# Performance work log

Measured on AMD Instinct MI355X. Metric: run time of the kernel, lower is better.

Reference implementation:

```python
import jax, jax.numpy as jnp
import numpy as np

N_NODES = 50000
N_EDGES = 600000
D_IN = 128
D_HID = 128
N_IDX = 4096


def gcn_conv(x, W, b, edge_index, num_nodes):
    """PyG GCNConv: add self loops, symmetric deg normalization, scatter-add, bias."""
    h = x @ W  # [N, D_out]
    loop = jnp.arange(num_nodes, dtype=edge_index.dtype)
    src = jnp.concatenate([edge_index[0], loop])
    dst = jnp.concatenate([edge_index[1], loop])
    deg = jax.ops.segment_sum(jnp.ones_like(dst, dtype=h.dtype), dst, num_segments=num_nodes)
    dinv = jnp.where(deg > 0, jax.lax.rsqrt(jnp.maximum(deg, 1.0)), 0.0)
    norm = dinv[src] * dinv[dst]  # [E+N]
    msgs = h[src] * norm[:, None]
    out = jax.ops.segment_sum(msgs, dst, num_segments=num_nodes)
    return out + b


def setup_inputs() -> dict:
    key = jax.random.key(0)
    ks = jax.random.split(key, 18)
    d = {
        "x": jax.random.normal(ks[0], (N_NODES, D_IN), dtype=jnp.float32),
        "syntactic_edge_index": jax.random.randint(ks[1], (2, N_EDGES), 0, N_NODES, dtype=jnp.int32),
        "sequential_edge_index": jax.random.randint(ks[2], (2, N_EDGES), 0, N_NODES, dtype=jnp.int32),
        "semantic_edge_index": jax.random.randint(ks[3], (2, N_EDGES), 0, N_NODES, dtype=jnp.int32),
        "index": jax.random.randint(ks[4], (N_IDX,), 0, N_NODES, dtype=jnp.int32),
    }
    s = 1.0 / np.sqrt(D_IN)
    names = ["syn", "seq", "sem"]
    for i, n in enumerate(names):
        d[f"w1_{n}"] = jax.random.uniform(ks[5 + i], (D_IN, D_HID), jnp.float32, -s, s)
        d[f"b1_{n}"] = jnp.zeros((D_HID,), jnp.float32)
        d[f"w2_{n}"] = jax.random.uniform(ks[8 + i], (D_HID, D_HID), jnp.float32, -s, s)
        d[f"b2_{n}"] = jnp.zeros((D_HID,), jnp.float32)
    return d


def reference(x, syntactic_edge_index, sequential_edge_index, semantic_edge_index, index,
              w1_syn, b1_syn, w1_seq, b1_seq, w1_sem, b1_sem,
              w2_syn, b2_syn, w2_seq, b2_seq, w2_sem, b2_sem):
    n = x.shape[0]
    # layer 1: three parallel GCN branches + ReLU (dropout is identity in eval mode)
    a = jax.nn.relu(gcn_conv(x, w1_syn, b1_syn, syntactic_edge_index, n))
    b = jax.nn.relu(gcn_conv(x, w1_seq, b1_seq, sequential_edge_index, n))
    c = jax.nn.relu(gcn_conv(x, w1_sem, b1_sem, semantic_edge_index, n))
    h = jnp.maximum(jnp.maximum(a, b), c)
    # layer 2
    a2 = jax.nn.relu(gcn_conv(h, w2_syn, b2_syn, syntactic_edge_index, n))
    b2 = jax.nn.relu(gcn_conv(h, w2_seq, b2_seq, sequential_edge_index, n))
    c2 = jax.nn.relu(gcn_conv(h, w2_sem, b2_sem, semantic_edge_index, n))
    out = jnp.maximum(jnp.maximum(a2, b2), c2)
    return out[index]
```

## Files before the change

kernel.cpp:

```cpp
#include <hip/hip_runtime.h>
#include <hip/hip_fp16.h>

#define NN 50000
#define NE 600000
#define NG 3
#define D  128
#define NI 4096
#define BW 1024
#define NBUCK 49
#define EPT_BIN 16
#define EPB_BIN (256 * EPT_BIN)
#define NBLK_BIN ((NE + EPB_BIN - 1) / EPB_BIN)
#define XCVT_BLKS 3125
#define WCVT_BLKS 48
#define CNT_BLKS (NBLK_BIN * NG)

typedef _Float16 half8 __attribute__((ext_vector_type(8)));
typedef _Float16 half4v __attribute__((ext_vector_type(4)));
typedef float floatx4 __attribute__((ext_vector_type(4)));

static __device__ __forceinline__ float wextract(unsigned int v) {
  unsigned short u = (unsigned short)(v >> 16);
  _Float16 h;
  __builtin_memcpy(&h, &u, 2);
  return (float)h;
}

static __device__ __forceinline__ unsigned int packsw(int s, float w) {
  _Float16 h = (_Float16)w;
  unsigned short u;
  __builtin_memcpy(&u, &h, 2);
  return (unsigned int)s | ((unsigned int)u << 16);
}


__global__ __launch_bounds__(256) void prep_kernel(
    const float* __restrict__ x, __half* __restrict__ xh,
    const float* __restrict__ W0, const float* __restrict__ W1, const float* __restrict__ W2,
    const float* __restrict__ W3, const float* __restrict__ W4, const float* __restrict__ W5,
    __half* __restrict__ Wf,
    const int* __restrict__ e0, const int* __restrict__ e1, const int* __restrict__ e2,
    int* __restrict__ bucketCnt) {
  __shared__ int cnt[NBUCK];
  int blk = blockIdx.x;
  int tid = threadIdx.x;
  if (blk < XCVT_BLKS) {
    int i = blk * 256 + tid;
    size_t base = (size_t)i * 8;
    float4 v0 = *(const float4*)&x[base];
    float4 v1 = *(const float4*)&x[base + 4];
    half8 h;
    h[0] = (_Float16)v0.x; h[1] = (_Float16)v0.y; h[2] = (_Float16)v0.z; h[3] = (_Float16)v0.w;
    h[4] = (_Float16)v1.x; h[5] = (_Float16)v1.y; h[6] = (_Float16)v1.z; h[7] = (_Float16)v1.w;
    *(half8*)&xh[base] = h;
  } else if (blk < XCVT_BLKS + WCVT_BLKS) {
    const float* Wm[6] = {W0, W1, W2, W3, W4, W5};
    int t = (blk - XCVT_BLKS) * 256 + tid;
    int mat = t >> 11;
    int fr = (t >> 6) & 31;
    int lane = t & 63;
    int tt = fr >> 2, ks = fr & 3;
    int n = tt * 16 + (lane & 15);
    int kb = ks * 32 + (lane >> 4) * 8;
    const float* W = Wm[mat];
#pragma unroll
    for (int j = 0; j < 8; j++)
      Wf[(size_t)t * 8 + j] = __float2half(W[(kb + j) * 128 + n]);
  } else {
    int cb = blk - XCVT_BLKS - WCVT_BLKS;
    int g = cb / NBLK_BIN, eb = cb % NBLK_BIN;
    const int* ei = (g == 0) ? e0 : ((g == 1) ? e1 : e2);
    if (tid < NBUCK) cnt[tid] = 0;
    __syncthreads();
    int base = eb * EPB_BIN;
#pragma unroll
    for (int i = 0; i < EPT_BIN; i++) {
      int e = base + tid + i * 256;
      if (e < NE) atomicAdd(&cnt[ei[NE + e] >> 10], 1);
    }
    __syncthreads();
    if (tid < NBUCK) atomicAdd(&bucketCnt[g * NBUCK + tid], cnt[tid]);
  }
}

__global__ void bscan_kernel(const int* __restrict__ bucketCnt, int* __restrict__ bucketBase,
                             int* __restrict__ cursor, int* __restrict__ rp) {
  int g = threadIdx.x >> 6;
  int lane = threadIdx.x & 63;
  if (g >= NG) return;
  int v = (lane < NBUCK) ? bucketCnt[g * NBUCK + lane] : 0;
  int incl = v;
#pragma unroll
  for (int off = 1; off < 64; off <<= 1) {
    int t = __shfl_up(incl, off, 64);
    if (lane >= off) incl += t;
  }
  int ex = incl - v;
  if (lane < NBUCK) {
    bucketBase[g * NBUCK + lane] = ex;
    cursor[g * NBUCK + lane] = ex;
  }
  if (lane == 0) rp[g * (NN + 1) + NN] = NE;
}

__global__ __launch_bounds__(256) void bin_kernel(const int* __restrict__ e0,
    const int* __restrict__ e1, const int* __restrict__ e2,
    int* __restrict__ cursor, unsigned int* __restrict__ binned) {
  __shared__ int cnt[4][NBUCK];
  __shared__ int base[NBUCK];
  __shared__ int woff[4][NBUCK];
  int g = blockIdx.y;
  const int* ei = (g == 0) ? e0 : ((g == 1) ? e1 : e2);
  int tid = threadIdx.x;
  int wave = tid >> 6;
  if (tid < NBUCK) { cnt[0][tid] = 0; cnt[1][tid] = 0; cnt[2][tid] = 0; cnt[3][tid] = 0; }
  __syncthreads();
  int estart = blockIdx.x * EPB_BIN;
  int src[EPT_BIN], dst[EPT_BIN], rk[EPT_BIN];
#pragma unroll
  for (int i = 0; i < EPT_BIN; i++) {
    int e = estart + tid + i * 256;
    if (e < NE) {
      src[i] = ei[e];
      dst[i] = ei[NE + e];
      rk[i] = atomicAdd(&cnt[wave][dst[i] >> 10], 1);
    } else {
      rk[i] = -1;
    }
  }
  __syncthreads();
  if (tid < NBUCK) {
    int c0 = cnt[0][tid], c1 = cnt[1][tid], c2 = cnt[2][tid], c3 = cnt[3][tid];
    int total = c0 + c1 + c2 + c3;
    base[tid] = (total > 0) ? atomicAdd(&cursor[g * NBUCK + tid], total) : 0;
    woff[0][tid] = 0; woff[1][tid] = c0; woff[2][tid] = c0 + c1; woff[3][tid] = c0 + c1 + c2;
  }
  __syncthreads();
#pragma unroll
  for (int i = 0; i < EPT_BIN; i++) {
    if (rk[i] >= 0) {
      int b = dst[i] >> 10;
      binned[(size_t)g * NE + base[b] + woff[wave][b] + rk[i]] =
          (unsigned int)src[i] | ((unsigned int)dst[i] << 16);
    }
  }
}

__global__ __launch_bounds__(256) void csr_kernel(const unsigned int* __restrict__ binned,
    const int* __restrict__ bucketBase, const int* __restrict__ bucketCnt,
    int* __restrict__ rp, float* __restrict__ dinv) {
  __shared__ int deg[BW];
  __shared__ int wsum[4];
  int g = blockIdx.y, b = blockIdx.x;
  int tid = threadIdx.x;
  int node0 = b * BW;
  int bb = bucketBase[g * NBUCK + b];
  int total = bucketCnt[g * NBUCK + b];
  const unsigned int* bp = binned + (size_t)g * NE + bb;
  for (int i = tid; i < BW; i += 256) deg[i] = 0;
  __syncthreads();
  for (int e = tid; e < total; e += 256) {
    unsigned int p = bp[e];
    atomicAdd(&deg[(int)(p >> 16) - node0], 1);
  }
  __syncthreads();
  int d0 = deg[tid * 4], d1 = deg[tid * 4 + 1], d2 = deg[tid * 4 + 2], d3 = deg[tid * 4 + 3];
  int s = d0 + d1 + d2 + d3;
  int lane = tid & 63;
  int incl = s;
#pragma unroll
  for (int off = 1; off < 64; off <<= 1) {
    int n = __shfl_up(incl, off, 64);
    if (lane >= off) incl += n;
  }
  if (lane == 63) wsum[tid >> 6] = incl;
  __syncthreads();
  int wbase = 0;
#pragma unroll
  for (int w = 0; w < 4; w++)
    if (w < (tid >> 6)) wbase += wsum[w];
  int ex = wbase + incl - s;
  int exs[4] = {ex, ex + d0, ex + d0 + d1, ex + d0 + d1 + d2};
  int ds[4] = {d0, d1, d2, d3};
#pragma unroll
  for (int k = 0; k < 4; k++) {
    int node = node0 + tid * 4 + k;
    if (node < NN) {
      rp[g * (NN + 1) + node] = bb + exs[k];
      dinv[g * NN + node] = rsqrtf((float)ds[k] + 1.0f);
    }
  }
}

__global__ __launch_bounds__(256) void fillp_kernel(const unsigned int* __restrict__ binned,
    const int* __restrict__ bucketBase, const int* __restrict__ bucketCnt,
    const int* __restrict__ rp, const float* __restrict__ dinv,
    unsigned int* __restrict__ colp) {
  __shared__ int cur[BW];
  int g = blockIdx.y, b = blockIdx.x;
  int tid = threadIdx.x;
  int node0 = b * BW;
  int bb = bucketBase[g * NBUCK + b];
  int total = bucketCnt[g * NBUCK + b];
  const unsigned int* bp = binned + (size_t)g * NE + bb;
  for (int i = tid; i < BW; i += 256) {
    int node = node0 + i;
    cur[i] = (node < NN) ? rp[g * (NN + 1) + node] : 0;
  }
  __syncthreads();
  for (int e = tid; e < total; e += 256) {
    unsigned int p = bp[e];
    int srcid = (int)(p & 0xffffu);
    int r = atomicAdd(&cur[(int)(p >> 16) - node0], 1);
    colp[(size_t)g * NE + r] = packsw(srcid, dinv[g * NN + srcid]);
  }
}


__global__ __launch_bounds__(256) void aggb_kernel(
    const __half* __restrict__ srch, const int* __restrict__ rp,
    const unsigned int* __restrict__ colp, const float* __restrict__ dinv,
    const int* __restrict__ index, __half* __restrict__ tout, int nrows) {
  int b = blockIdx.y;
  int w = (blockIdx.x * 256 + threadIdx.x) >> 6;
  if (w >= nrows) return;
  int lane = threadIdx.x & 63;
  int sub = lane >> 5;
  int fl = lane & 31;
  int node = index ? index[w] : w;
  const _Float16* srcv = (const _Float16*)srch;
  half4v selfh = *(const half4v*)&srcv[(size_t)node * D + fl * 4];
  float di = dinv[b * NN + node];
  float a[4];
#pragma unroll
  for (int k = 0; k < 4; k++) a[k] = sub ? 0.f : di * (float)selfh[k];
  const int* rpb = rp + b * (NN + 1);
  int s = rpb[node], e = rpb[node + 1];
  int n = e - s;
  const unsigned int* cp = colp + (size_t)b * NE;
  unsigned int c = (lane < n) ? cp[s + lane] : 0u;
  int m = min(n, 64);
  for (int j = 0; j < m; j += 8) {
    half4v h[4];
    float wg[4];
#pragma unroll
    for (int u = 0; u < 4; u++) {
      unsigned int v = (unsigned int)__shfl((int)c, j + u * 2 + sub, 64);
      wg[u] = wextract(v);
      h[u] = *(const half4v*)&srcv[(size_t)(v & 0xffffu) * D + fl * 4];
    }
#pragma unroll
    for (int u = 0; u < 4; u++)
#pragma unroll
      for (int k = 0; k < 4; k++) a[k] = fmaf((float)h[u][k], wg[u], a[k]);
  }
  for (int q = s + 64; q < e; q += 64) {
    int nn = min(e - q, 64);
    unsigned int cc = (lane < nn) ? cp[q + lane] : 0u;
    for (int j = 0; j < nn; j += 2) {
      unsigned int v = (unsigned int)__shfl((int)cc, j + sub, 64);
      float wf = wextract(v);
      half4v hv = *(const half4v*)&srcv[(size_t)(v & 0xffffu) * D + fl * 4];
#pragma unroll
      for (int k = 0; k < 4; k++) a[k] = fmaf((float)hv[k], wf, a[k]);
    }
  }
#pragma unroll
  for (int k = 0; k < 4; k++) a[k] += __shfl_xor(a[k], 32, 64);
  if (sub == 0) {
    half4v o;
#pragma unroll
    for (int k = 0; k < 4; k++) o[k] = (_Float16)(di * a[k]);
    _Float16* tv = (_Float16*)tout;
    *(half4v*)&tv[(size_t)b * nrows * D + (size_t)w * D + fl * 4] = o;
  }
}


#define ALD 136

__global__ __launch_bounds__(256) void mmf_kernel(const __half* __restrict__ A,
    const __half* __restrict__ Wf,
    const float* __restrict__ B0, const float* __restrict__ B1, const float* __restrict__ B2,
    __half* __restrict__ outh, float* __restrict__ outf, int M) {
  __shared__ _Float16 As[128 * ALD];
  __shared__ _Float16 Ws[16384];
  const float* Bb[3] = {B0, B1, B2};
  const int tid = threadIdx.x;
  const int wave = tid >> 6, lane = tid & 63;
  const int wr = (wave >> 1) * 64, wc = (wave & 1) * 64;
  const int ln = lane & 15, quad = lane >> 4;
  const int row0 = blockIdx.x * 128;
  float om[4][4][4];

  for (int b = 0; b < 3; b++) {
    const __half* Wb = Wf + (size_t)b * 16384;
#pragma unroll
    for (int i = 0; i < 8; i++) {
      int id = tid + i * 256;
      *(half8*)&Ws[id * 8] = *(const half8*)&Wb[(size_t)id * 8];
    }
    const __half* Ab = A + (size_t)b * M * D;
#pragma unroll
    for (int i = 0; i < 8; i++) {
      int idx = tid + i * 256;
      int r = idx >> 4, c8 = idx & 15;
      int gr = row0 + r;
      gr = (gr < M) ? gr : (M - 1);
      half8 v = *(const half8*)&Ab[(size_t)gr * D + c8 * 8];
      *(half8*)&As[r * ALD + c8 * 8] = v;
    }
    __syncthreads();

    float bias[4];
#pragma unroll
    for (int ct = 0; ct < 4; ct++) bias[ct] = Bb[b][wc + ct * 16 + ln];
    floatx4 acc[4][4];
#pragma unroll
    for (int rt = 0; rt < 4; rt++)
#pragma unroll
      for (int ct = 0; ct < 4; ct++)
        acc[rt][ct] = (floatx4){bias[ct], bias[ct], bias[ct], bias[ct]};

#pragma unroll
    for (int ks = 0; ks < 4; ks++) {
      half8 av[4];
#pragma unroll
      for (int rt = 0; rt < 4; rt++)
        av[rt] = *(const half8*)&As[(wr + rt * 16 + ln) * ALD + ks * 32 + quad * 8];
#pragma unroll
      for (int ct = 0; ct < 4; ct++) {
        int tt = (wc >> 4) + ct;
        half8 bv = *(const half8*)&Ws[((tt * 4 + ks) * 64 + lane) * 8];
#pragma unroll
        for (int rt = 0; rt < 4; rt++)
          acc[rt][ct] = __builtin_amdgcn_mfma_f32_16x16x32_f16(av[rt], bv, acc[rt][ct], 0, 0, 0);
      }
    }
#pragma unroll
    for (int rt = 0; rt < 4; rt++)
#pragma unroll
      for (int ct = 0; ct < 4; ct++)
#pragma unroll
        for (int r = 0; r < 4; r++) {
          float v = fmaxf(acc[rt][ct][r], 0.f);
          om[rt][ct][r] = (b == 0) ? v : fmaxf(om[rt][ct][r], v);
        }
    __syncthreads();
  }
#pragma unroll
  for (int rt = 0; rt < 4; rt++) {
    int m = row0 + wr + rt * 16 + quad * 4;
#pragma unroll
    for (int r = 0; r < 4; r++) {
      if (m + r < M) {
#pragma unroll
        for (int ct = 0; ct < 4; ct++) {
          int n = wc + ct * 16 + ln;
          if (outh) outh[(size_t)(m + r) * D + n] = __float2half(om[rt][ct][r]);
          else      outf[(size_t)(m + r) * D + n] = om[rt][ct][r];
        }
      }
    }
  }
}


extern "C" void kernel_launch(void* const* d_in, const int* in_sizes, int n_in,
                              void* d_out, int out_size, void* d_ws, size_t ws_size,
                              hipStream_t stream) {
  const float* x = (const float*)d_in[0];
  const int* e0 = (const int*)d_in[1];
  const int* e1 = (const int*)d_in[2];
  const int* e2 = (const int*)d_in[3];
  const int* index = (const int*)d_in[4];
  const float* w1[3] = {(const float*)d_in[5], (const float*)d_in[9],  (const float*)d_in[13]};
  const float* b1[3] = {(const float*)d_in[6], (const float*)d_in[10], (const float*)d_in[14]};
  const float* w2[3] = {(const float*)d_in[7], (const float*)d_in[11], (const float*)d_in[15]};
  const float* b2[3] = {(const float*)d_in[8], (const float*)d_in[12], (const float*)d_in[16]};
  float* out = (float*)d_out;

  char* ws = (char*)d_ws;
  size_t o = 0;
  auto alloc = [&](size_t bytes) {
    o = (o + 255) & ~(size_t)255;
    void* p = ws + o;
    o += bytes;
    return p;
  };
  int*    rp     = (int*)alloc((size_t)NG * (NN + 1) * 4);
  unsigned int* colp = (unsigned int*)alloc((size_t)NG * NE * 4);
  float*  dinv   = (float*)alloc((size_t)NG * NN * 4);
  int*    bcnt   = (int*)alloc((size_t)NG * NBUCK * 4);
  int*    bbase  = (int*)alloc((size_t)NG * NBUCK * 4);
  int*    bcur   = (int*)alloc((size_t)NG * NBUCK * 4);
  __half* xh     = (__half*)alloc((size_t)NN * D * 2);
  __half* Wf     = (__half*)alloc((size_t)6 * 128 * 128 * 2);
  __half* t1     = (__half*)alloc((size_t)NG * NN * D * 2);
  __half* hacc   = (__half*)alloc((size_t)NN * D * 2);
  unsigned int* binned = (unsigned int*)t1;
  __half* t2     = t1;
  (void)ws_size; (void)in_sizes; (void)n_in; (void)out_size;

  hipMemsetAsync(bcnt, 0, (size_t)NG * NBUCK * 4, stream);
  prep_kernel<<<XCVT_BLKS + WCVT_BLKS + CNT_BLKS, 256, 0, stream>>>(
      x, xh, w1[0], w1[1], w1[2], w2[0], w2[1], w2[2], Wf, e0, e1, e2, bcnt);
  bscan_kernel<<<1, 192, 0, stream>>>(bcnt, bbase, bcur, rp);
  bin_kernel<<<dim3(NBLK_BIN, NG), 256, 0, stream>>>(e0, e1, e2, bcur, binned);
  csr_kernel<<<dim3(NBUCK, NG), 256, 0, stream>>>(binned, bbase, bcnt, rp, dinv);
  fillp_kernel<<<dim3(NBUCK, NG), 256, 0, stream>>>(binned, bbase, bcnt, rp, dinv, colp);

  aggb_kernel<<<dim3((NN * 64 + 255) / 256, NG), 256, 0, stream>>>(
      xh, rp, colp, dinv, nullptr, t1, NN);
  mmf_kernel<<<(NN + 127) / 128, 256, 0, stream>>>(t1, Wf, b1[0], b1[1], b1[2],
                                                   hacc, nullptr, NN);
  aggb_kernel<<<dim3((NI * 64 + 255) / 256, NG), 256, 0, stream>>>(
      hacc, rp, colp, dinv, index, t2, NI);
  mmf_kernel<<<(NI + 127) / 128, 256, 0, stream>>>(t2, Wf + (size_t)3 * 16384,
                                                   b2[0], b2[1], b2[2], nullptr, out, NI);
}
```

Measured before the change: 278.0 us.

## Fold bucket scan into consumer kernels and widen aggregation gather batch

Result: no change. 279.1 us (+0.4%).

```diff
diff --git a/kernel.cpp b/kernel.cpp
--- a/kernel.cpp
+++ b/kernel.cpp
@@ -31,6 +31,17 @@
   unsigned short u;
   __builtin_memcpy(&u, &h, 2);
   return (unsigned int)s | ((unsigned int)u << 16);
+}
+
+static __device__ __forceinline__ int bucket_scan(const int* bcnt, int g, int lane) {
+  int v = (lane < NBUCK) ? bcnt[g * NBUCK + lane] : 0;
+  int incl = v;
+#pragma unroll
+  for (int off = 1; off < 64; off <<= 1) {
+    int t = __shfl_up(incl, off, 64);
+    if (lane >= off) incl += t;
+  }
+  return incl - v;
 }
 
 
@@ -83,36 +94,22 @@
   }
 }
 
-__global__ void bscan_kernel(const int* __restrict__ bucketCnt, int* __restrict__ bucketBase,
-                             int* __restrict__ cursor, int* __restrict__ rp) {
-  int g = threadIdx.x >> 6;
-  int lane = threadIdx.x & 63;
-  if (g >= NG) return;
-  int v = (lane < NBUCK) ? bucketCnt[g * NBUCK + lane] : 0;
-  int incl = v;
-#pragma unroll
-  for (int off = 1; off < 64; off <<= 1) {
-    int t = __shfl_up(incl, off, 64);
-    if (lane >= off) incl += t;
-  }
-  int ex = incl - v;
-  if (lane < NBUCK) {
-    bucketBase[g * NBUCK + lane] = ex;
-    cursor[g * NBUCK + lane] = ex;
-  }
-  if (lane == 0) rp[g * (NN + 1) + NN] = NE;
-}
-
 __global__ __launch_bounds__(256) void bin_kernel(const int* __restrict__ e0,
     const int* __restrict__ e1, const int* __restrict__ e2,
-    int* __restrict__ cursor, unsigned int* __restrict__ binned) {
+    const int* __restrict__ bcnt, int* __restrict__ cur0,
+    unsigned int* __restrict__ binned) {
   __shared__ int cnt[4][NBUCK];
+  __shared__ int sbase[NBUCK];
   __shared__ int base[NBUCK];
   __shared__ int woff[4][NBUCK];
   int g = blockIdx.y;
   const int* ei = (g == 0) ? e0 : ((g == 1) ? e1 : e2);
   int tid = threadIdx.x;
   int wave = tid >> 6;
+  if (tid < 64) {
+    int ex = bucket_scan(bcnt, g, tid);
+    if (tid < NBUCK) sbase[tid] = ex;
+  }
   if (tid < NBUCK) { cnt[0][tid] = 0; cnt[1][tid] = 0; cnt[2][tid] = 0; cnt[3][tid] = 0; }
   __syncthreads();
   int estart = blockIdx.x * EPB_BIN;
@@ -132,7 +129,8 @@
   if (tid < NBUCK) {
     int c0 = cnt[0][tid], c1 = cnt[1][tid], c2 = cnt[2][tid], c3 = cnt[3][tid];
     int total = c0 + c1 + c2 + c3;
-    base[tid] = (total > 0) ? atomicAdd(&cursor[g * NBUCK + tid], total) : 0;
+    int wb = (total > 0) ? atomicAdd(&cur0[g * NBUCK + tid], total) : 0;
+    base[tid] = sbase[tid] + wb;
     woff[0][tid] = 0; woff[1][tid] = c0; woff[2][tid] = c0 + c1; woff[3][tid] = c0 + c1 + c2;
   }
   __syncthreads();
@@ -147,18 +145,23 @@
 }
 
 __global__ __launch_bounds__(256) void csr_kernel(const unsigned int* __restrict__ binned,
-    const int* __restrict__ bucketBase, const int* __restrict__ bucketCnt,
-    int* __restrict__ rp, float* __restrict__ dinv) {
+    const int* __restrict__ bcnt, int* __restrict__ rp, float* __restrict__ dinv) {
   __shared__ int deg[BW];
   __shared__ int wsum[4];
+  __shared__ int sbb;
   int g = blockIdx.y, b = blockIdx.x;
   int tid = threadIdx.x;
   int node0 = b * BW;
-  int bb = bucketBase[g * NBUCK + b];
-  int total = bucketCnt[g * NBUCK + b];
+  if (tid < 64) {
+    int ex = bucket_scan(bcnt, g, tid);
+    if (tid == b) sbb = ex;
+  }
+  if (b == 0 && tid == 0) rp[g * (NN + 1) + NN] = NE;
+  for (int i = tid; i < BW; i += 256) deg[i] = 0;
+  __syncthreads();
+  int bb = sbb;
+  int total = bcnt[g * NBUCK + b];
   const unsigned int* bp = binned + (size_t)g * NE + bb;
-  for (int i = tid; i < BW; i += 256) deg[i] = 0;
-  __syncthreads();
   for (int e = tid; e < total; e += 256) {
     unsigned int p = bp[e];
     atomicAdd(&deg[(int)(p >> 16) - node0], 1);
@@ -193,21 +196,25 @@
 }
 
 __global__ __launch_bounds__(256) void fillp_kernel(const unsigned int* __restrict__ binned,
-    const int* __restrict__ bucketBase, const int* __restrict__ bucketCnt,
-    const int* __restrict__ rp, const float* __restrict__ dinv,
-    unsigned int* __restrict__ colp) {
+    const int* __restrict__ bcnt, const int* __restrict__ rp,
+    const float* __restrict__ dinv, unsigned int* __restrict__ colp) {
   __shared__ int cur[BW];
+  __shared__ int sbb;
   int g = blockIdx.y, b = blockIdx.x;
   int tid = threadIdx.x;
   int node0 = b * BW;
-  int bb = bucketBase[g * NBUCK + b];
-  int total = bucketCnt[g * NBUCK + b];
-  const unsigned int* bp = binned + (size_t)g * NE + bb;
+  if (tid < 64) {
+    int ex = bucket_scan(bcnt, g, tid);
+    if (tid == b) sbb = ex;
+  }
   for (int i = tid; i < BW; i += 256) {
     int node = node0 + i;
     cur[i] = (node < NN) ? rp[g * (NN + 1) + node] : 0;
   }
   __syncthreads();
+  int bb = sbb;
+  int total = bcnt[g * NBUCK + b];
+  const unsigned int* bp = binned + (size_t)g * NE + bb;
   for (int e = tid; e < total; e += 256) {
     unsigned int p = bp[e];
     int srcid = (int)(p & 0xffffu);
@@ -240,17 +247,18 @@
   const unsigned int* cp = colp + (size_t)b * NE;
   unsigned int c = (lane < n) ? cp[s + lane] : 0u;
   int m = min(n, 64);
-  for (int j = 0; j < m; j += 8) {
-    half4v h[4];
-    float wg[4];
-#pragma unroll
-    for (int u = 0; u < 4; u++) {
-      unsigned int v = (unsigned int)__shfl((int)c, j + u * 2 + sub, 64);
-      wg[u] = wextract(v);
-      h[u] = *(const half4v*)&srcv[(size_t)(v & 0xffffu) * D + fl * 4];
-    }
-#pragma unroll
-    for (int u = 0; u < 4; u++)
+  for (int j = 0; j < m; j += 16) {
+    unsigned int v[8];
+    float wg[8];
+    half4v h[8];
+#pragma unroll
+    for (int u = 0; u < 8; u++) {
+      v[u] = (unsigned int)__shfl((int)c, j + u * 2 + sub, 64);
+      wg[u] = wextract(v[u]);
+      h[u] = *(const half4v*)&srcv[(size_t)(v[u] & 0xffffu) * D + fl * 4];
+    }
+#pragma unroll
+    for (int u = 0; u < 8; u++)
 #pragma unroll
       for (int k = 0; k < 4; k++) a[k] = fmaf((float)h[u][k], wg[u], a[k]);
   }
@@ -391,9 +399,8 @@
   int*    rp     = (int*)alloc((size_t)NG * (NN + 1) * 4);
   unsigned int* colp = (unsigned int*)alloc((size_t)NG * NE * 4);
   float*  dinv   = (float*)alloc((size_t)NG * NN * 4);
-  int*    bcnt   = (int*)alloc((size_t)NG * NBUCK * 4);
-  int*    bbase  = (int*)alloc((size_t)NG * NBUCK * 4);
-  int*    bcur   = (int*)alloc((size_t)NG * NBUCK * 4);
+  int*    bcnt   = (int*)alloc((size_t)2 * NG * NBUCK * 4);
+  int*    cur0   = bcnt + NG * NBUCK;
   __half* xh     = (__half*)alloc((size_t)NN * D * 2);
   __half* Wf     = (__half*)alloc((size_t)6 * 128 * 128 * 2);
   __half* t1     = (__half*)alloc((size_t)NG * NN * D * 2);
@@ -402,13 +409,12 @@
   __half* t2     = t1;
   (void)ws_size; (void)in_sizes; (void)n_in; (void)out_size;
 
-  hipMemsetAsync(bcnt, 0, (size_t)NG * NBUCK * 4, stream);
+  hipMemsetAsync(bcnt, 0, (size_t)2 * NG * NBUCK * 4, stream);
   prep_kernel<<<XCVT_BLKS + WCVT_BLKS + CNT_BLKS, 256, 0, stream>>>(
       x, xh, w1[0], w1[1], w1[2], w2[0], w2[1], w2[2], Wf, e0, e1, e2, bcnt);
-  bscan_kernel<<<1, 192, 0, stream>>>(bcnt, bbase, bcur, rp);
-  bin_kernel<<<dim3(NBLK_BIN, NG), 256, 0, stream>>>(e0, e1, e2, bcur, binned);
-  csr_kernel<<<dim3(NBUCK, NG), 256, 0, stream>>>(binned, bbase, bcnt, rp, dinv);
-  fillp_kernel<<<dim3(NBUCK, NG), 256, 0, stream>>>(binned, bbase, bcnt, rp, dinv, colp);
+  bin_kernel<<<dim3(NBLK_BIN, NG), 256, 0, stream>>>(e0, e1, e2, bcnt, cur0, binned);
+  csr_kernel<<<dim3(NBUCK, NG), 256, 0, stream>>>(binned, bcnt, rp, dinv);
+  fillp_kernel<<<dim3(NBUCK, NG), 256, 0, stream>>>(binned, bcnt, rp, dinv, colp);
 
   aggb_kernel<<<dim3((NN * 64 + 255) / 256, NG), 256, 0, stream>>>(
       xh, rp, colp, dinv, nullptr, t1, NN);
```
